# Kernel tuning notes

Hardware: AMD Instinct MI355X
Metric: run time of the kernel (lower is better)

Reference implementation:

```python
import jax, jax.numpy as jnp
import numpy as np

N = 50000   # nodes
E = 512000  # edges
D = 64      # embedding_dim
L = 4       # num_layers
ATOM_DIMS = np.array([119, 5, 12, 12, 10, 6, 6, 2, 2])  # OGB atom feature vocab sizes
BOND_DIMS = np.array([5, 6, 2])                          # OGB bond feature vocab sizes


def _ln(x, g, b, eps=1e-5):
    m = x.mean(-1, keepdims=True)
    v = x.var(-1, keepdims=True)
    return (x - m) * jax.lax.rsqrt(v + eps) * g + b


def setup_inputs() -> dict:
    key = jax.random.key(0)
    ks = jax.random.split(key, 12)
    s = 0.05
    x = jax.random.randint(ks[0], (N, 9), 0, jnp.asarray(ATOM_DIMS)[None, :])
    edge_attr = jax.random.randint(ks[1], (E, 3), 0, jnp.asarray(BOND_DIMS)[None, :])
    edge_index = jax.random.randint(ks[2], (2, E), 0, N)
    # padded embedding tables: [n_feats, max_vocab, D]
    atom_emb = jax.random.normal(ks[3], (9, 119, D), jnp.float32) * s
    bond_emb = jax.random.normal(ks[4], (3, 6, D), jnp.float32) * s
    eps = jnp.zeros((L,), jnp.float32)  # GIN eps, init 0
    W1 = jax.random.normal(ks[5], (L, D, 2 * D), jnp.float32) * s
    b1 = jnp.zeros((L, 2 * D), jnp.float32)
    W2 = jax.random.normal(ks[6], (L, 2 * D, D), jnp.float32) * s
    b2 = jnp.zeros((L, D), jnp.float32)
    ln_g = jnp.ones((L, D), jnp.float32)
    ln_b = jnp.zeros((L, D), jnp.float32)
    Wu1 = jax.random.normal(ks[7], (L, 3 * D, 3 * D), jnp.float32) * s
    bu1 = jnp.zeros((L, 3 * D), jnp.float32)
    ug = jnp.ones((L, 3 * D), jnp.float32)
    ub = jnp.zeros((L, 3 * D), jnp.float32)
    Wu2 = jax.random.normal(ks[8], (L, 3 * D, D), jnp.float32) * s
    bu2 = jnp.zeros((L, D), jnp.float32)
    return dict(x=x, edge_attr=edge_attr, edge_index=edge_index,
                atom_emb=atom_emb, bond_emb=bond_emb, eps=eps,
                W1=W1, b1=b1, W2=W2, b2=b2, ln_g=ln_g, ln_b=ln_b,
                Wu1=Wu1, bu1=bu1, ug=ug, ub=ub, Wu2=Wu2, bu2=bu2)


def reference(x, edge_attr, edge_index, atom_emb, bond_emb, eps,
              W1, b1, W2, b2, ln_g, ln_b, Wu1, bu1, ug, ub, Wu2, bu2):
    # Atom/Bond encoders: sum of per-column categorical embeddings
    node = atom_emb[jnp.arange(9)[None, :], x].sum(axis=1)       # [N, D]
    edge = bond_emb[jnp.arange(3)[None, :], edge_attr].sum(axis=1)  # [E, D]
    src, dst = edge_index[0], edge_index[1]
    for l in range(L):
        # MyGINConv (GINE): aggregate relu(x_src + e) at dst, mlp((1+eps)x + agg)
        msg = jax.nn.relu(node[src] + edge)                      # [E, D]
        agg = jax.ops.segment_sum(msg, dst, num_segments=N)      # [N, D]
        h = (1.0 + eps[l]) * node + agg
        h = jax.nn.relu(h @ W1[l] + b1[l]) @ W2[l] + b2[l]       # conv MLP
        h = _ln(h, ln_g[l], ln_b[l])                             # batch_norms[l] (LayerNorm)
        node = jax.nn.relu(h) + node                             # dropout=identity (eval) + residual
        # SparseEdgeUpdateLayer (residual=True)
        cat = jnp.concatenate([node[src], node[dst], edge], axis=-1)  # [E, 3D]
        m = _ln(cat @ Wu1[l] + bu1[l], ug[l], ub[l])
        edge = jax.nn.relu(m) @ Wu2[l] + bu2[l] + edge
    return node, edge
```

## Files before the change

### kernel.cpp

```cpp
#include <hip/hip_runtime.h>
#include <hip/hip_bf16.h>


#define GIN_N 50000
#define GIN_E 512000

typedef __attribute__((ext_vector_type(8))) short short8;
typedef __attribute__((ext_vector_type(4))) float f32x4;
typedef unsigned short u16;

__device__ __forceinline__ u16 bf16r(float x) {
    unsigned u = __builtin_bit_cast(unsigned, x);
    u += 0x7fffu + ((u >> 16) & 1u);
    return (u16)(u >> 16);
}
__device__ __forceinline__ float bf16f(u16 h) {
    unsigned u = ((unsigned)h) << 16;
    return __builtin_bit_cast(float, u);
}

__global__ __launch_bounds__(256) void zero_f32(float* __restrict__ p, int n) {
    int i = blockIdx.x * 256 + threadIdx.x;
    if (i < n) p[i] = 0.f;
}

__global__ __launch_bounds__(256) void atom_encode(const int* __restrict__ x,
        const float* __restrict__ emb, float* __restrict__ node, int N) {
    int idx = blockIdx.x * 256 + threadIdx.x;
    int n = idx >> 6, lane = idx & 63;
    if (n >= N) return;
    float s = 0.f;
#pragma unroll
    for (int f = 0; f < 9; ++f) {
        int v = x[n * 9 + f];
        s += emb[(f * 119 + v) * 64 + lane];
    }
    node[(size_t)n * 64 + lane] = s;
}

__global__ __launch_bounds__(256) void bond_encode(const int* __restrict__ ea,
        const float* __restrict__ emb, float* __restrict__ edge, int E) {
    int idx = blockIdx.x * 256 + threadIdx.x;
    int e = idx >> 6, lane = idx & 63;
    if (e >= E) return;
    float s = 0.f;
#pragma unroll
    for (int f = 0; f < 3; ++f) {
        int v = ea[e * 3 + f];
        s += emb[(f * 6 + v) * 64 + lane];
    }
    edge[(size_t)e * 64 + lane] = s;
}

__global__ __launch_bounds__(256) void msg_scatter(const int* __restrict__ src,
        const int* __restrict__ dst, const float* __restrict__ node,
        const float* __restrict__ edge, float* __restrict__ agg, int E) {
    int idx = blockIdx.x * 256 + threadIdx.x;
    int e = idx >> 6, lane = idx & 63;
    if (e >= E) return;
    int s = src[e], d = dst[e];
    float v = node[(size_t)s * 64 + lane] + edge[(size_t)e * 64 + lane];
    v = fmaxf(v, 0.f);
    unsafeAtomicAdd(&agg[(size_t)d * 64 + lane], v);
}

__global__ __launch_bounds__(256) void pack_b1(const float* __restrict__ W,
        u16* __restrict__ out, int K, int Nc, int F) {
    int tid = blockIdx.x * 256 + threadIdx.x;
    int lane = tid & 63;
    int frag = (tid >> 6) % F;
    int layer = tid / (F * 64);
    int tpr = Nc / 16;
    int ks = frag / tpr, tt = frag % tpr;
    int k0 = ks * 32 + ((lane >> 4) << 3);
    int col = tt * 16 + (lane & 15);
    const float* w = W + (size_t)layer * K * Nc;
    u16* o = out + ((size_t)layer * F + frag) * 512 + (size_t)lane * 8;
#pragma unroll
    for (int j = 0; j < 8; ++j) o[j] = bf16r(w[(size_t)(k0 + j) * Nc + col]);
}
__global__ __launch_bounds__(256) void pack_b2(const float* __restrict__ W,
        u16* __restrict__ out, int K, int Nc, int F) {
    int tid = blockIdx.x * 256 + threadIdx.x;
    int lane = tid & 63;
    int frag = (tid >> 6) % F;
    int layer = tid / (F * 64);
    int tpr = Nc / 16;
    int ks = frag / tpr, tt = frag % tpr;
    int k0 = ks * 32 + ((lane >> 4) << 3);
    int col = tt * 16 + (lane & 15);
    const float* w = W + (size_t)layer * K * Nc;
    u16* o = out + ((size_t)layer * F + frag) * 1024 + (size_t)lane * 8;
#pragma unroll
    for (int j = 0; j < 8; ++j) {
        float v = w[(size_t)(k0 + j) * Nc + col];
        u16 hi = bf16r(v);
        o[j] = hi;
        o[512 + j] = bf16r(v - bf16f(hi));
    }
}

__global__ __launch_bounds__(256, 2) void node_mlp(
        const float* __restrict__ nodeIn, float* __restrict__ nodeOut,
        float* __restrict__ agg,
        const float* __restrict__ epsArr, int l,
        const u16* __restrict__ pw1, const u16* __restrict__ pw2,
        const float* __restrict__ b1, const float* __restrict__ b2,
        const float* __restrict__ lng, const float* __restrict__ lnb, int N) {
    __shared__ u16 xH[64][72], xL[64][72];
    __shared__ u16 hH[64][136], hL[64][136];
    __shared__ float pS[4][64], pS2[4][64], lnM[64], lnR[64];
    const int t = threadIdx.x, w = t >> 6, lane = t & 63;
    const int g = lane >> 4, c0 = lane & 15;
    const float epf = 1.f + epsArr[l];

#pragma unroll
    for (int i = 0; i < 16; ++i) {
        int r = w * 16 + i;
        int n = blockIdx.x * 64 + r;
        float x = 0.f;
        if (n < N) {
            size_t o = (size_t)n * 64 + lane;
            x = epf * nodeIn[o] + agg[o];
            agg[o] = 0.f;
        }
        u16 h = bf16r(x);
        xH[r][lane] = h;
        xL[r][lane] = bf16r(x - bf16f(h));
    }
    __syncthreads();

    f32x4 a1[4][2];
#pragma unroll
    for (int sp = 0; sp < 4; ++sp)
#pragma unroll
        for (int lt = 0; lt < 2; ++lt) a1[sp][lt] = (f32x4)0.f;
#pragma unroll
    for (int ks = 0; ks < 2; ++ks) {
        short8 aH[4], aL[4];
#pragma unroll
        for (int sp = 0; sp < 4; ++sp) {
            aH[sp] = *(const short8*)&xH[sp * 16 + c0][ks * 32 + g * 8];
            aL[sp] = *(const short8*)&xL[sp * 16 + c0][ks * 32 + g * 8];
        }
#pragma unroll
        for (int lt = 0; lt < 2; ++lt) {
            const u16* p = pw1 + (size_t)(ks * 8 + w * 2 + lt) * 1024 + (size_t)lane * 8;
            short8 bH = *(const short8*)p;
            short8 bL = *(const short8*)(p + 512);
#pragma unroll
            for (int sp = 0; sp < 4; ++sp) {
                a1[sp][lt] = __builtin_amdgcn_mfma_f32_16x16x32_bf16(aH[sp], bH, a1[sp][lt], 0, 0, 0);
                a1[sp][lt] = __builtin_amdgcn_mfma_f32_16x16x32_bf16(aH[sp], bL, a1[sp][lt], 0, 0, 0);
                a1[sp][lt] = __builtin_amdgcn_mfma_f32_16x16x32_bf16(aL[sp], bH, a1[sp][lt], 0, 0, 0);
            }
        }
    }
#pragma unroll
    for (int lt = 0; lt < 2; ++lt) {
        int col = w * 32 + lt * 16 + c0;
        float bias = b1[col];
#pragma unroll
        for (int sp = 0; sp < 4; ++sp)
#pragma unroll
            for (int rg = 0; rg < 4; ++rg) {
                int r = sp * 16 + g * 4 + rg;
                float v = fmaxf(a1[sp][lt][rg] + bias, 0.f);
                u16 h = bf16r(v);
                hH[r][col] = h;
                hL[r][col] = bf16r(v - bf16f(h));
            }
    }
    __syncthreads();

    f32x4 a2[4];
#pragma unroll
    for (int sp = 0; sp < 4; ++sp) a2[sp] = (f32x4)0.f;
#pragma unroll
    for (int ks = 0; ks < 4; ++ks) {
        const u16* p = pw2 + (size_t)(ks * 4 + w) * 1024 + (size_t)lane * 8;
        short8 bH = *(const short8*)p;
        short8 bL = *(const short8*)(p + 512);
#pragma unroll
        for (int sp = 0; sp < 4; ++sp) {
            short8 aH = *(const short8*)&hH[sp * 16 + c0][ks * 32 + g * 8];
            short8 aL = *(const short8*)&hL[sp * 16 + c0][ks * 32 + g * 8];
            a2[sp] = __builtin_amdgcn_mfma_f32_16x16x32_bf16(aH, bH, a2[sp], 0, 0, 0);
            a2[sp] = __builtin_amdgcn_mfma_f32_16x16x32_bf16(aH, bL, a2[sp], 0, 0, 0);
            a2[sp] = __builtin_amdgcn_mfma_f32_16x16x32_bf16(aL, bH, a2[sp], 0, 0, 0);
        }
    }
    float bias2 = b2[w * 16 + c0];
    float s1v[4][4], s2v[4][4];
#pragma unroll
    for (int sp = 0; sp < 4; ++sp)
#pragma unroll
        for (int rg = 0; rg < 4; ++rg) {
            float v = a2[sp][rg] + bias2;
            a2[sp][rg] = v;
            s1v[sp][rg] = v;
            s2v[sp][rg] = v * v;
        }
#pragma unroll
    for (int off = 1; off < 16; off <<= 1)
#pragma unroll
        for (int sp = 0; sp < 4; ++sp)
#pragma unroll
            for (int rg = 0; rg < 4; ++rg) {
                s1v[sp][rg] += __shfl_xor(s1v[sp][rg], off);
                s2v[sp][rg] += __shfl_xor(s2v[sp][rg], off);
            }
    if (c0 == 0) {
#pragma unroll
        for (int sp = 0; sp < 4; ++sp)
#pragma unroll
            for (int rg = 0; rg < 4; ++rg) {
                int r = sp * 16 + g * 4 + rg;
                pS[w][r] = s1v[sp][rg];
                pS2[w][r] = s2v[sp][rg];
            }
    }
    __syncthreads();
    if (t < 64) {
        float a = pS[0][t] + pS[1][t] + pS[2][t] + pS[3][t];
        float b = pS2[0][t] + pS2[1][t] + pS2[2][t] + pS2[3][t];
        float mean = a * (1.f / 64.f);
        float var = b * (1.f / 64.f) - mean * mean;
        lnM[t] = mean;
        lnR[t] = rsqrtf(var + 1e-5f);
    }
    __syncthreads();

    int col = w * 16 + c0;
    float gg = lng[col], bc = lnb[col];
#pragma unroll
    for (int sp = 0; sp < 4; ++sp)
#pragma unroll
        for (int rg = 0; rg < 4; ++rg) {
            int r = sp * 16 + g * 4 + rg;
            int n = blockIdx.x * 64 + r;
            if (n < N) {
                float y = (a2[sp][rg] - lnM[r]) * lnR[r] * gg + bc;
                float xold = nodeIn[(size_t)n * 64 + col];
                nodeOut[(size_t)n * 64 + col] = fmaxf(y, 0.f) + xold;
            }
        }
}

template <bool SCATTER>
__global__ __launch_bounds__(256, 4) void edge_update_v4(
        const int* __restrict__ src, const int* __restrict__ dst,
        const float* __restrict__ node, float* __restrict__ edge,
        float* __restrict__ agg,
        const u16* __restrict__ pb1, const u16* __restrict__ pb2,
        const float* __restrict__ bu1, const float* __restrict__ ug,
        const float* __restrict__ ub, const float* __restrict__ bu2) {
    __shared__ u16 cat[64][200];
    __shared__ float pS[4][64], pS2[4][64];
    __shared__ float lnM[64], lnR[64];
    const int t = threadIdx.x, w = t >> 6, lane = t & 63;
    const int g = lane >> 4, c0 = lane & 15;
    const long eB = (long)blockIdx.x * 64;

#pragma unroll
    for (int i = 0; i < 16; ++i) {
        int r = w * 16 + i;
        long ge = eB + r;
        int s = src[ge], d = dst[ge];
        cat[r][lane]       = bf16r(node[(size_t)s * 64 + lane]);
        cat[r][64 + lane]  = bf16r(node[(size_t)d * 64 + lane]);
        cat[r][128 + lane] = bf16r(edge[(size_t)ge * 64 + lane]);
    }
    __syncthreads();

    f32x4 acc[4][3];
#pragma unroll
    for (int sp = 0; sp < 4; ++sp)
#pragma unroll
        for (int lt = 0; lt < 3; ++lt) acc[sp][lt] = (f32x4)0.f;
#pragma unroll
    for (int ks = 0; ks < 6; ++ks) {
        short8 a[4];
#pragma unroll
        for (int sp = 0; sp < 4; ++sp)
            a[sp] = *(const short8*)&cat[sp * 16 + c0][ks * 32 + g * 8];
#pragma unroll
        for (int lt = 0; lt < 3; ++lt) {
            const u16* p = pb1 + (size_t)(ks * 12 + w * 3 + lt) * 512 + (size_t)lane * 8;
            short8 b = *(const short8*)p;
#pragma unroll
            for (int sp = 0; sp < 4; ++sp)
                acc[sp][lt] = __builtin_amdgcn_mfma_f32_16x16x32_bf16(a[sp], b, acc[sp][lt], 0, 0, 0);
        }
    }

    float bs[3];
#pragma unroll
    for (int lt = 0; lt < 3; ++lt) bs[lt] = bu1[w * 48 + lt * 16 + c0];
    float s1v[4][4], s2v[4][4];
#pragma unroll
    for (int sp = 0; sp < 4; ++sp)
#pragma unroll
        for (int rg = 0; rg < 4; ++rg) { s1v[sp][rg] = 0.f; s2v[sp][rg] = 0.f; }
#pragma unroll
    for (int sp = 0; sp < 4; ++sp)
#pragma unroll
        for (int lt = 0; lt < 3; ++lt)
#pragma unroll
            for (int rg = 0; rg < 4; ++rg) {
                float v = acc[sp][lt][rg] + bs[lt];
                acc[sp][lt][rg] = v;
                s1v[sp][rg] += v;
                s2v[sp][rg] += v * v;
            }
#pragma unroll
    for (int off = 1; off < 16; off <<= 1)
#pragma unroll
        for (int sp = 0; sp < 4; ++sp)
#pragma unroll
            for (int rg = 0; rg < 4; ++rg) {
                s1v[sp][rg] += __shfl_xor(s1v[sp][rg], off);
                s2v[sp][rg] += __shfl_xor(s2v[sp][rg], off);
            }
    if (c0 == 0) {
#pragma unroll
        for (int sp = 0; sp < 4; ++sp)
#pragma unroll
            for (int rg = 0; rg < 4; ++rg) {
                int r = sp * 16 + g * 4 + rg;
                pS[w][r] = s1v[sp][rg];
                pS2[w][r] = s2v[sp][rg];
            }
    }
    __syncthreads();
    if (t < 64) {
        float a = pS[0][t] + pS[1][t] + pS[2][t] + pS[3][t];
        float b = pS2[0][t] + pS2[1][t] + pS2[2][t] + pS2[3][t];
        float mean = a * (1.f / 192.f);
        float var = b * (1.f / 192.f) - mean * mean;
        lnM[t] = mean;
        lnR[t] = rsqrtf(var + 1e-5f);
    }
    __syncthreads();

#pragma unroll
    for (int lt = 0; lt < 3; ++lt) {
        int col = w * 48 + lt * 16 + c0;
        float gg = ug[col], bb = ub[col];
#pragma unroll
        for (int sp = 0; sp < 4; ++sp)
#pragma unroll
            for (int rg = 0; rg < 4; ++rg) {
                int r = sp * 16 + g * 4 + rg;
                float v = (acc[sp][lt][rg] - lnM[r]) * lnR[r] * gg + bb;
                cat[r][col] = bf16r(fmaxf(v, 0.f));
            }
    }
    __syncthreads();

    f32x4 a2[4];
#pragma unroll
    for (int sp = 0; sp < 4; ++sp) a2[sp] = (f32x4)0.f;
#pragma unroll
    for (int ks = 0; ks < 6; ++ks) {
        const u16* p = pb2 + (size_t)(ks * 4 + w) * 512 + (size_t)lane * 8;
        short8 b = *(const short8*)p;
#pragma unroll
        for (int sp = 0; sp < 4; ++sp) {
            short8 a = *(const short8*)&cat[sp * 16 + c0][ks * 32 + g * 8];
            a2[sp] = __builtin_amdgcn_mfma_f32_16x16x32_bf16(a, b, a2[sp], 0, 0, 0);
        }
    }
    const int col = w * 16 + c0;
    float bb2 = bu2[col];
#pragma unroll
    for (int sp = 0; sp < 4; ++sp)
#pragma unroll
        for (int rg = 0; rg < 4; ++rg) {
            int r = sp * 16 + g * 4 + rg;
            long ge = eB + r;
            size_t off = (size_t)ge * 64 + col;
            float eNew = a2[sp][rg] + bb2 + edge[off];
            edge[off] = eNew;
            if (SCATTER) {
                int s = src[ge];
                float ns = node[(size_t)s * 64 + col];
                float msg = fmaxf(ns + eNew, 0.f);
                int dd = dst[ge];
                unsafeAtomicAdd(&agg[(size_t)dd * 64 + col], msg);
            }
        }
}

extern "C" void kernel_launch(void* const* d_in, const int* in_sizes, int n_in,
                              void* d_out, int out_size, void* d_ws, size_t ws_size,
                              hipStream_t stream) {
    const int*   x         = (const int*)d_in[0];
    const int*   edge_attr = (const int*)d_in[1];
    const int*   edge_index= (const int*)d_in[2];
    const float* atom_emb  = (const float*)d_in[3];
    const float* bond_emb  = (const float*)d_in[4];
    const float* eps       = (const float*)d_in[5];
    const float* W1        = (const float*)d_in[6];
    const float* b1        = (const float*)d_in[7];
    const float* W2        = (const float*)d_in[8];
    const float* b2        = (const float*)d_in[9];
    const float* ln_g      = (const float*)d_in[10];
    const float* ln_b      = (const float*)d_in[11];
    const float* Wu1       = (const float*)d_in[12];
    const float* bu1       = (const float*)d_in[13];
    const float* ug        = (const float*)d_in[14];
    const float* ub        = (const float*)d_in[15];
    const float* Wu2       = (const float*)d_in[16];
    const float* bu2       = (const float*)d_in[17];

    const int N = GIN_N, E = GIN_E;
    const int* src = edge_index;
    const int* dst = edge_index + E;

    float* node = (float*)d_out;
    float* edge = (float*)d_out + (size_t)N * 64;

    char* ws = (char*)d_ws;
    float* nodeAlt = (float*)ws;  ws += (size_t)N * 64 * 4;
    float* agg     = (float*)ws;  ws += (size_t)N * 64 * 4;
    u16* pb1       = (u16*)ws;    ws += (size_t)4 * 72 * 512 * 2;
    u16* pb2       = (u16*)ws;    ws += (size_t)4 * 24 * 512 * 2;
    u16* pw1       = (u16*)ws;    ws += (size_t)4 * 16 * 1024 * 2;
    u16* pw2       = (u16*)ws;    ws += (size_t)4 * 16 * 1024 * 2;

    pack_b1<<<(4 * 72 * 64) / 256, 256, 0, stream>>>(Wu1, pb1, 192, 192, 72);
    pack_b1<<<(4 * 24 * 64) / 256, 256, 0, stream>>>(Wu2, pb2, 192, 64, 24);
    pack_b2<<<(4 * 16 * 64) / 256, 256, 0, stream>>>(W1, pw1, 64, 128, 16);
    pack_b2<<<(4 * 16 * 64) / 256, 256, 0, stream>>>(W2, pw2, 128, 64, 16);

    atom_encode<<<(N * 64 + 255) / 256, 256, 0, stream>>>(x, atom_emb, node, N);
    bond_encode<<<(E * 64) / 256, 256, 0, stream>>>(edge_attr, bond_emb, edge, E);

    zero_f32<<<(N * 64) / 256, 256, 0, stream>>>(agg, N * 64);
    msg_scatter<<<(E * 64) / 256, 256, 0, stream>>>(src, dst, node, edge, agg, E);

    const int nodeBlocks = (N + 63) / 64;
    for (int l = 0; l < 4; ++l) {
        const float* nIn  = (l & 1) ? nodeAlt : node;
        float*       nOut = (l & 1) ? node    : nodeAlt;
        node_mlp<<<nodeBlocks, 256, 0, stream>>>(nIn, nOut, agg, eps, l,
            pw1 + (size_t)l * 16 * 1024, pw2 + (size_t)l * 16 * 1024,
            b1 + (size_t)l * 128, b2 + (size_t)l * 64,
            ln_g + (size_t)l * 64, ln_b + (size_t)l * 64, N);
        if (l < 3)
            edge_update_v4<true><<<E / 64, 256, 0, stream>>>(src, dst, nOut, edge, agg,
                pb1 + (size_t)l * 72 * 512, pb2 + (size_t)l * 24 * 512,
                bu1 + (size_t)l * 192,
                ug + (size_t)l * 192, ub + (size_t)l * 192,
                bu2 + (size_t)l * 64);
        else
            edge_update_v4<false><<<E / 64, 256, 0, stream>>>(src, dst, nOut, edge, agg,
                pb1 + (size_t)l * 72 * 512, pb2 + (size_t)l * 24 * 512,
                bu1 + (size_t)l * 192,
                ug + (size_t)l * 192, ub + (size_t)l * 192,
                bu2 + (size_t)l * 64);
    }
}
```

Baseline: 989.2 us.

## Restructure edge update to per-wave 16-edge tiles with bf16 node copy

Each wave now owns 16 edges and computes all 192 columns of the first GEMM itself. A-fragments are loaded straight from global memory into registers, and LayerNorm statistics come from lane shuffles. This removes the shared-memory staging of the concatenated inputs and all block-wide __syncthreads. The node MLP additionally writes a bf16 copy of node features so the edge gathers read half the bytes. The bond encoder is also fused with the initial message scatter, saving one pass over the edge tensor. The trade-off is that each wave re-reads the whole Wu1 fragment set, and more accumulator registers are live per wave, which may lower occupancy.

After: 1.043 ms. 5.4% more time.

```diff
diff --git a/kernel.cpp b/kernel.cpp
--- a/kernel.cpp
+++ b/kernel.cpp
@@ -17,6 +17,14 @@
 __device__ __forceinline__ float bf16f(u16 h) {
     unsigned u = ((unsigned)h) << 16;
     return __builtin_bit_cast(float, u);
+}
+__device__ __forceinline__ short8 cvt8(float4 u, float4 v) {
+    short8 r;
+    r[0] = (short)bf16r(u.x); r[1] = (short)bf16r(u.y);
+    r[2] = (short)bf16r(u.z); r[3] = (short)bf16r(u.w);
+    r[4] = (short)bf16r(v.x); r[5] = (short)bf16r(v.y);
+    r[6] = (short)bf16r(v.z); r[7] = (short)bf16r(v.w);
+    return r;
 }
 
 __global__ __launch_bounds__(256) void zero_f32(float* __restrict__ p, int n) {
@@ -38,8 +46,11 @@
     node[(size_t)n * 64 + lane] = s;
 }
 
-__global__ __launch_bounds__(256) void bond_encode(const int* __restrict__ ea,
-        const float* __restrict__ emb, float* __restrict__ edge, int E) {
+__global__ __launch_bounds__(256) void bond_encode_scatter(
+        const int* __restrict__ ea, const float* __restrict__ emb,
+        float* __restrict__ edge, const int* __restrict__ src,
+        const int* __restrict__ dst, const float* __restrict__ node,
+        float* __restrict__ agg, int E) {
     int idx = blockIdx.x * 256 + threadIdx.x;
     int e = idx >> 6, lane = idx & 63;
     if (e >= E) return;
@@ -50,18 +61,9 @@
         s += emb[(f * 6 + v) * 64 + lane];
     }
     edge[(size_t)e * 64 + lane] = s;
-}
-
-__global__ __launch_bounds__(256) void msg_scatter(const int* __restrict__ src,
-        const int* __restrict__ dst, const float* __restrict__ node,
-        const float* __restrict__ edge, float* __restrict__ agg, int E) {
-    int idx = blockIdx.x * 256 + threadIdx.x;
-    int e = idx >> 6, lane = idx & 63;
-    if (e >= E) return;
-    int s = src[e], d = dst[e];
-    float v = node[(size_t)s * 64 + lane] + edge[(size_t)e * 64 + lane];
-    v = fmaxf(v, 0.f);
-    unsafeAtomicAdd(&agg[(size_t)d * 64 + lane], v);
+    int si = src[e], di = dst[e];
+    float msg = fmaxf(node[(size_t)si * 64 + lane] + s, 0.f);
+    unsafeAtomicAdd(&agg[(size_t)di * 64 + lane], msg);
 }
 
 __global__ __launch_bounds__(256) void pack_b1(const float* __restrict__ W,
@@ -102,7 +104,7 @@
 
 __global__ __launch_bounds__(256, 2) void node_mlp(
         const float* __restrict__ nodeIn, float* __restrict__ nodeOut,
-        float* __restrict__ agg,
+        u16* __restrict__ nodeB, float* __restrict__ agg,
         const float* __restrict__ epsArr, int l,
         const u16* __restrict__ pw1, const u16* __restrict__ pw2,
         const float* __restrict__ b1, const float* __restrict__ b2,
@@ -242,154 +244,129 @@
             if (n < N) {
                 float y = (a2[sp][rg] - lnM[r]) * lnR[r] * gg + bc;
                 float xold = nodeIn[(size_t)n * 64 + col];
-                nodeOut[(size_t)n * 64 + col] = fmaxf(y, 0.f) + xold;
+                float out = fmaxf(y, 0.f) + xold;
+                nodeOut[(size_t)n * 64 + col] = out;
+                nodeB[(size_t)n * 64 + col] = bf16r(out);
             }
         }
 }
 
 template <bool SCATTER>
-__global__ __launch_bounds__(256, 4) void edge_update_v4(
+__global__ __launch_bounds__(256, 4) void edge_update_v5(
         const int* __restrict__ src, const int* __restrict__ dst,
-        const float* __restrict__ node, float* __restrict__ edge,
-        float* __restrict__ agg,
+        const float* __restrict__ node, const u16* __restrict__ nodeB,
+        float* __restrict__ edge, float* __restrict__ agg,
         const u16* __restrict__ pb1, const u16* __restrict__ pb2,
         const float* __restrict__ bu1, const float* __restrict__ ug,
         const float* __restrict__ ub, const float* __restrict__ bu2) {
-    __shared__ u16 cat[64][200];
-    __shared__ float pS[4][64], pS2[4][64];
-    __shared__ float lnM[64], lnR[64];
+    __shared__ u16 mld[4][16][200];
     const int t = threadIdx.x, w = t >> 6, lane = t & 63;
     const int g = lane >> 4, c0 = lane & 15;
-    const long eB = (long)blockIdx.x * 64;
-
-#pragma unroll
-    for (int i = 0; i < 16; ++i) {
-        int r = w * 16 + i;
-        long ge = eB + r;
-        int s = src[ge], d = dst[ge];
-        cat[r][lane]       = bf16r(node[(size_t)s * 64 + lane]);
-        cat[r][64 + lane]  = bf16r(node[(size_t)d * 64 + lane]);
-        cat[r][128 + lane] = bf16r(edge[(size_t)ge * 64 + lane]);
-    }
-    __syncthreads();
-
-    f32x4 acc[4][3];
-#pragma unroll
-    for (int sp = 0; sp < 4; ++sp)
-#pragma unroll
-        for (int lt = 0; lt < 3; ++lt) acc[sp][lt] = (f32x4)0.f;
+    const int eB16 = (blockIdx.x * 4 + w) * 16;
+
+    const int eRow = eB16 + c0;
+    const int sI = src[eRow], dI = dst[eRow];
+    const u16* nsrow = nodeB + (size_t)sI * 64;
+    const u16* ndrow = nodeB + (size_t)dI * 64;
+    const float* erow = edge + (size_t)eRow * 64;
+    short8 a[6];
+    a[0] = *(const short8*)(nsrow + g * 8);
+    a[1] = *(const short8*)(nsrow + 32 + g * 8);
+    a[2] = *(const short8*)(ndrow + g * 8);
+    a[3] = *(const short8*)(ndrow + 32 + g * 8);
+    {
+        float4 e0 = *(const float4*)(erow + g * 8);
+        float4 e1 = *(const float4*)(erow + g * 8 + 4);
+        float4 e2 = *(const float4*)(erow + 32 + g * 8);
+        float4 e3 = *(const float4*)(erow + 32 + g * 8 + 4);
+        a[4] = cvt8(e0, e1);
+        a[5] = cvt8(e2, e3);
+    }
+
+    f32x4 acc1[12];
+#pragma unroll
+    for (int lt = 0; lt < 12; ++lt) acc1[lt] = (f32x4)0.f;
+#pragma unroll
+    for (int lt = 0; lt < 12; ++lt) {
+#pragma unroll
+        for (int ks = 0; ks < 6; ++ks) {
+            const u16* p = pb1 + (size_t)(ks * 12 + lt) * 512 + (size_t)lane * 8;
+            short8 b = *(const short8*)p;
+            acc1[lt] = __builtin_amdgcn_mfma_f32_16x16x32_bf16(a[ks], b, acc1[lt], 0, 0, 0);
+        }
+    }
+
+    float s1[4] = {0.f, 0.f, 0.f, 0.f}, s2[4] = {0.f, 0.f, 0.f, 0.f};
+#pragma unroll
+    for (int lt = 0; lt < 12; ++lt) {
+        float bias = bu1[lt * 16 + c0];
+#pragma unroll
+        for (int rg = 0; rg < 4; ++rg) {
+            float v = acc1[lt][rg] + bias;
+            acc1[lt][rg] = v;
+            s1[rg] += v;
+            s2[rg] += v * v;
+        }
+    }
+#pragma unroll
+    for (int off = 1; off < 16; off <<= 1)
+#pragma unroll
+        for (int rg = 0; rg < 4; ++rg) {
+            s1[rg] += __shfl_xor(s1[rg], off);
+            s2[rg] += __shfl_xor(s2[rg], off);
+        }
+    float mean[4], rs[4];
+#pragma unroll
+    for (int rg = 0; rg < 4; ++rg) {
+        mean[rg] = s1[rg] * (1.f / 192.f);
+        float var = s2[rg] * (1.f / 192.f) - mean[rg] * mean[rg];
+        rs[rg] = rsqrtf(var + 1e-5f);
+    }
+
+#pragma unroll
+    for (int lt = 0; lt < 12; ++lt) {
+        int col = lt * 16 + c0;
+        float gg = ug[col], bb = ub[col];
+#pragma unroll
+        for (int rg = 0; rg < 4; ++rg) {
+            float v = (acc1[lt][rg] - mean[rg]) * rs[rg] * gg + bb;
+            mld[w][g * 4 + rg][col] = bf16r(fmaxf(v, 0.f));
+        }
+    }
+    asm volatile("s_waitcnt lgkmcnt(0)" ::: "memory");
+    __builtin_amdgcn_sched_barrier(0);
+
+    f32x4 acc2[4];
+#pragma unroll
+    for (int lt = 0; lt < 4; ++lt) acc2[lt] = (f32x4)0.f;
 #pragma unroll
     for (int ks = 0; ks < 6; ++ks) {
-        short8 a[4];
-#pragma unroll
-        for (int sp = 0; sp < 4; ++sp)
-            a[sp] = *(const short8*)&cat[sp * 16 + c0][ks * 32 + g * 8];
-#pragma unroll
-        for (int lt = 0; lt < 3; ++lt) {
-            const u16* p = pb1 + (size_t)(ks * 12 + w * 3 + lt) * 512 + (size_t)lane * 8;
+        short8 av = *(const short8*)&mld[w][c0][ks * 32 + g * 8];
+#pragma unroll
+        for (int lt = 0; lt < 4; ++lt) {
+            const u16* p = pb2 + (size_t)(ks * 4 + lt) * 512 + (size_t)lane * 8;
             short8 b = *(const short8*)p;
-#pragma unroll
-            for (int sp = 0; sp < 4; ++sp)
-                acc[sp][lt] = __builtin_amdgcn_mfma_f32_16x16x32_bf16(a[sp], b, acc[sp][lt], 0, 0, 0);
-        }
-    }
-
-    float bs[3];
-#pragma unroll
-    for (int lt = 0; lt < 3; ++lt) bs[lt] = bu1[w * 48 + lt * 16 + c0];
-    float s1v[4][4], s2v[4][4];
-#pragma unroll
-    for (int sp = 0; sp < 4; ++sp)
-#pragma unroll
-        for (int rg = 0; rg < 4; ++rg) { s1v[sp][rg] = 0.f; s2v[sp][rg] = 0.f; }
-#pragma unroll
-    for (int sp = 0; sp < 4; ++sp)
-#pragma unroll
-        for (int lt = 0; lt < 3; ++lt)
-#pragma unroll
-            for (int rg = 0; rg < 4; ++rg) {
-                float v = acc[sp][lt][rg] + bs[lt];
-                acc[sp][lt][rg] = v;
-                s1v[sp][rg] += v;
-                s2v[sp][rg] += v * v;
-            }
-#pragma unroll
-    for (int off = 1; off < 16; off <<= 1)
-#pragma unroll
-        for (int sp = 0; sp < 4; ++sp)
-#pragma unroll
-            for (int rg = 0; rg < 4; ++rg) {
-                s1v[sp][rg] += __shfl_xor(s1v[sp][rg], off);
-                s2v[sp][rg] += __shfl_xor(s2v[sp][rg], off);
-            }
-    if (c0 == 0) {
-#pragma unroll
-        for (int sp = 0; sp < 4; ++sp)
-#pragma unroll
-            for (int rg = 0; rg < 4; ++rg) {
-                int r = sp * 16 + g * 4 + rg;
-                pS[w][r] = s1v[sp][rg];
-                pS2[w][r] = s2v[sp][rg];
-            }
-    }
-    __syncthreads();
-    if (t < 64) {
-        float a = pS[0][t] + pS[1][t] + pS[2][t] + pS[3][t];
-        float b = pS2[0][t] + pS2[1][t] + pS2[2][t] + pS2[3][t];
-        float mean = a * (1.f / 192.f);
-        float var = b * (1.f / 192.f) - mean * mean;
-        lnM[t] = mean;
-        lnR[t] = rsqrtf(var + 1e-5f);
-    }
-    __syncthreads();
-
-#pragma unroll
-    for (int lt = 0; lt < 3; ++lt) {
-        int col = w * 48 + lt * 16 + c0;
-        float gg = ug[col], bb = ub[col];
-#pragma unroll
-        for (int sp = 0; sp < 4; ++sp)
-#pragma unroll
-            for (int rg = 0; rg < 4; ++rg) {
-                int r = sp * 16 + g * 4 + rg;
-                float v = (acc[sp][lt][rg] - lnM[r]) * lnR[r] * gg + bb;
-                cat[r][col] = bf16r(fmaxf(v, 0.f));
-            }
-    }
-    __syncthreads();
-
-    f32x4 a2[4];
-#pragma unroll
-    for (int sp = 0; sp < 4; ++sp) a2[sp] = (f32x4)0.f;
-#pragma unroll
-    for (int ks = 0; ks < 6; ++ks) {
-        const u16* p = pb2 + (size_t)(ks * 4 + w) * 512 + (size_t)lane * 8;
-        short8 b = *(const short8*)p;
-#pragma unroll
-        for (int sp = 0; sp < 4; ++sp) {
-            short8 a = *(const short8*)&cat[sp * 16 + c0][ks * 32 + g * 8];
-            a2[sp] = __builtin_amdgcn_mfma_f32_16x16x32_bf16(a, b, a2[sp], 0, 0, 0);
-        }
-    }
-    const int col = w * 16 + c0;
-    float bb2 = bu2[col];
-#pragma unroll
-    for (int sp = 0; sp < 4; ++sp)
-#pragma unroll
-        for (int rg = 0; rg < 4; ++rg) {
-            int r = sp * 16 + g * 4 + rg;
-            long ge = eB + r;
-            size_t off = (size_t)ge * 64 + col;
-            float eNew = a2[sp][rg] + bb2 + edge[off];
+            acc2[lt] = __builtin_amdgcn_mfma_f32_16x16x32_bf16(av, b, acc2[lt], 0, 0, 0);
+        }
+    }
+
+#pragma unroll
+    for (int rg = 0; rg < 4; ++rg) {
+        int e = eB16 + g * 4 + rg;
+        int sI2 = 0, dI2 = 0;
+        if (SCATTER) { sI2 = src[e]; dI2 = dst[e]; }
+#pragma unroll
+        for (int lt = 0; lt < 4; ++lt) {
+            int col = lt * 16 + c0;
+            size_t off = (size_t)e * 64 + col;
+            float eNew = acc2[lt][rg] + bu2[col] + edge[off];
             edge[off] = eNew;
             if (SCATTER) {
-                int s = src[ge];
-                float ns = node[(size_t)s * 64 + col];
-                float msg = fmaxf(ns + eNew, 0.f);
-                int dd = dst[ge];
-                unsafeAtomicAdd(&agg[(size_t)dd * 64 + col], msg);
-            }
-        }
+                float msg = fmaxf(node[(size_t)sI2 * 64 + col] + eNew, 0.f);
+                unsafeAtomicAdd(&agg[(size_t)dI2 * 64 + col], msg);
+            }
+        }
+    }
 }
 
 extern "C" void kernel_launch(void* const* d_in, const int* in_sizes, int n_in,
@@ -424,6 +401,7 @@
     char* ws = (char*)d_ws;
     float* nodeAlt = (float*)ws;  ws += (size_t)N * 64 * 4;
     float* agg     = (float*)ws;  ws += (size_t)N * 64 * 4;
+    u16*   nodeB   = (u16*)ws;    ws += (size_t)N * 64 * 2;
     u16* pb1       = (u16*)ws;    ws += (size_t)4 * 72 * 512 * 2;
     u16* pb2       = (u16*)ws;    ws += (size_t)4 * 24 * 512 * 2;
     u16* pw1       = (u16*)ws;    ws += (size_t)4 * 16 * 1024 * 2;
@@ -435,27 +413,28 @@
     pack_b2<<<(4 * 16 * 64) / 256, 256, 0, stream>>>(W2, pw2, 128, 64, 16);
 
     atom_encode<<<(N * 64 + 255) / 256, 256, 0, stream>>>(x, atom_emb, node, N);
-    bond_encode<<<(E * 64) / 256, 256, 0, stream>>>(edge_attr, bond_emb, edge, E);
-
     zero_f32<<<(N * 64) / 256, 256, 0, stream>>>(agg, N * 64);
-    msg_scatter<<<(E * 64) / 256, 256, 0, stream>>>(src, dst, node, edge, agg, E);
+    bond_encode_scatter<<<(E * 64) / 256, 256, 0, stream>>>(edge_attr, bond_emb,
+        edge, src, dst, node, agg, E);
 
     const int nodeBlocks = (N + 63) / 64;
     for (int l = 0; l < 4; ++l) {
         const float* nIn  = (l & 1) ? nodeAlt : node;
         float*       nOut = (l & 1) ? node    : nodeAlt;
-        node_mlp<<<nodeBlocks, 256, 0, stream>>>(nIn, nOut, agg, eps, l,
+        node_mlp<<<nodeBlocks, 256, 0, stream>>>(nIn, nOut, nodeB, agg, eps, l,
             pw1 + (size_t)l * 16 * 1024, pw2 + (size_t)l * 16 * 1024,
             b1 + (size_t)l * 128, b2 + (size_t)l * 64,
             ln_g + (size_t)l * 64, ln_b + (size_t)l * 64, N);
         if (l < 3)
-            edge_update_v4<true><<<E / 64, 256, 0, stream>>>(src, dst, nOut, edge, agg,
+            edge_update_v5<true><<<E / 64, 256, 0, stream>>>(src, dst, nOut, nodeB,
+                edge, agg,
                 pb1 + (size_t)l * 72 * 512, pb2 + (size_t)l * 24 * 512,
                 bu1 + (size_t)l * 192,
                 ug + (size_t)l * 192, ub + (size_t)l * 192,
                 bu2 + (size_t)l * 64);
         else
-            edge_update_v4<false><<<E / 64, 256, 0, stream>>>(src, dst, nOut, edge, agg,
+            edge_update_v5<false><<<E / 64, 256, 0, stream>>>(src, dst, nOut, nodeB,
+                edge, agg,
                 pb1 + (size_t)l * 72 * 512, pb2 + (size_t)l * 24 * 512,
                 bu1 + (size_t)l * 192,
                 ug + (size_t)l * 192, ub + (size_t)l * 192,
```

## Store edge and node state in bf16 and fuse bond encode with first scatter

Applied to the files above, without the earlier changes.

Keeps the running edge embedding in a bf16 workspace buffer and writes the fp32 edge output only in the last layer. Node_mlp also writes a bf16 copy of the node state so the edge kernel gathers 2-byte rows instead of converting fp32. Bond encoding is fused with the first message scatter, and the node ping-pong buffer is replaced by in-place updates. This roughly halves gather and edge read/write traffic. The cost is that the residual edge path now accumulates in bf16 across layers, which loses precision relative to the fp32 reference.

New measurement: 912.7 us. 1.08x faster.

```diff
diff --git a/kernel.cpp b/kernel.cpp
--- a/kernel.cpp
+++ b/kernel.cpp
@@ -38,8 +38,11 @@
     node[(size_t)n * 64 + lane] = s;
 }
 
-__global__ __launch_bounds__(256) void bond_encode(const int* __restrict__ ea,
-        const float* __restrict__ emb, float* __restrict__ edge, int E) {
+__global__ __launch_bounds__(256) void bond_encode_scatter(
+        const int* __restrict__ ea, const float* __restrict__ emb,
+        u16* __restrict__ edgeB, const int* __restrict__ src,
+        const int* __restrict__ dst, const float* __restrict__ node,
+        float* __restrict__ agg, int E) {
     int idx = blockIdx.x * 256 + threadIdx.x;
     int e = idx >> 6, lane = idx & 63;
     if (e >= E) return;
@@ -49,19 +52,10 @@
         int v = ea[e * 3 + f];
         s += emb[(f * 6 + v) * 64 + lane];
     }
-    edge[(size_t)e * 64 + lane] = s;
-}
-
-__global__ __launch_bounds__(256) void msg_scatter(const int* __restrict__ src,
-        const int* __restrict__ dst, const float* __restrict__ node,
-        const float* __restrict__ edge, float* __restrict__ agg, int E) {
-    int idx = blockIdx.x * 256 + threadIdx.x;
-    int e = idx >> 6, lane = idx & 63;
-    if (e >= E) return;
-    int s = src[e], d = dst[e];
-    float v = node[(size_t)s * 64 + lane] + edge[(size_t)e * 64 + lane];
-    v = fmaxf(v, 0.f);
-    unsafeAtomicAdd(&agg[(size_t)d * 64 + lane], v);
+    edgeB[(size_t)e * 64 + lane] = bf16r(s);
+    int si = src[e], di = dst[e];
+    float msg = fmaxf(node[(size_t)si * 64 + lane] + s, 0.f);
+    unsafeAtomicAdd(&agg[(size_t)di * 64 + lane], msg);
 }
 
 __global__ __launch_bounds__(256) void pack_b1(const float* __restrict__ W,
@@ -101,7 +95,7 @@
 }
 
 __global__ __launch_bounds__(256, 2) void node_mlp(
-        const float* __restrict__ nodeIn, float* __restrict__ nodeOut,
+        float* __restrict__ node, u16* __restrict__ nodeB,
         float* __restrict__ agg,
         const float* __restrict__ epsArr, int l,
         const u16* __restrict__ pw1, const u16* __restrict__ pw2,
@@ -121,7 +115,7 @@
         float x = 0.f;
         if (n < N) {
             size_t o = (size_t)n * 64 + lane;
-            x = epf * nodeIn[o] + agg[o];
+            x = epf * node[o] + agg[o];
             agg[o] = 0.f;
         }
         u16 h = bf16r(x);
@@ -240,22 +234,26 @@
             int r = sp * 16 + g * 4 + rg;
             int n = blockIdx.x * 64 + r;
             if (n < N) {
+                size_t o = (size_t)n * 64 + col;
                 float y = (a2[sp][rg] - lnM[r]) * lnR[r] * gg + bc;
-                float xold = nodeIn[(size_t)n * 64 + col];
-                nodeOut[(size_t)n * 64 + col] = fmaxf(y, 0.f) + xold;
+                float out = fmaxf(y, 0.f) + node[o];
+                node[o] = out;
+                nodeB[o] = bf16r(out);
             }
         }
 }
 
 template <bool SCATTER>
-__global__ __launch_bounds__(256, 4) void edge_update_v4(
+__global__ __launch_bounds__(256, 4) void edge_update_v6(
         const int* __restrict__ src, const int* __restrict__ dst,
-        const float* __restrict__ node, float* __restrict__ edge,
+        const float* __restrict__ node, const u16* __restrict__ nodeB,
+        u16* __restrict__ edgeB, float* __restrict__ edgeF,
         float* __restrict__ agg,
         const u16* __restrict__ pb1, const u16* __restrict__ pb2,
         const float* __restrict__ bu1, const float* __restrict__ ug,
         const float* __restrict__ ub, const float* __restrict__ bu2) {
-    __shared__ u16 cat[64][200];
+    __shared__ u16 cat[64][202];
+    __shared__ u16 eold[64][66];
     __shared__ float pS[4][64], pS2[4][64];
     __shared__ float lnM[64], lnR[64];
     const int t = threadIdx.x, w = t >> 6, lane = t & 63;
@@ -267,9 +265,11 @@
         int r = w * 16 + i;
         long ge = eB + r;
         int s = src[ge], d = dst[ge];
-        cat[r][lane]       = bf16r(node[(size_t)s * 64 + lane]);
-        cat[r][64 + lane]  = bf16r(node[(size_t)d * 64 + lane]);
-        cat[r][128 + lane] = bf16r(edge[(size_t)ge * 64 + lane]);
+        cat[r][lane]       = nodeB[(size_t)s * 64 + lane];
+        cat[r][64 + lane]  = nodeB[(size_t)d * 64 + lane];
+        u16 ev = edgeB[(size_t)ge * 64 + lane];
+        cat[r][128 + lane] = ev;
+        eold[r][lane] = ev;
     }
     __syncthreads();
 
@@ -371,23 +371,23 @@
             a2[sp] = __builtin_amdgcn_mfma_f32_16x16x32_bf16(a, b, a2[sp], 0, 0, 0);
         }
     }
+
     const int col = w * 16 + c0;
-    float bb2 = bu2[col];
+    const float bb2 = bu2[col];
 #pragma unroll
     for (int sp = 0; sp < 4; ++sp)
 #pragma unroll
         for (int rg = 0; rg < 4; ++rg) {
             int r = sp * 16 + g * 4 + rg;
             long ge = eB + r;
-            size_t off = (size_t)ge * 64 + col;
-            float eNew = a2[sp][rg] + bb2 + edge[off];
-            edge[off] = eNew;
+            float eNew = a2[sp][rg] + bb2 + bf16f(eold[r][col]);
             if (SCATTER) {
-                int s = src[ge];
-                float ns = node[(size_t)s * 64 + col];
-                float msg = fmaxf(ns + eNew, 0.f);
-                int dd = dst[ge];
-                unsafeAtomicAdd(&agg[(size_t)dd * 64 + col], msg);
+                edgeB[(size_t)ge * 64 + col] = bf16r(eNew);
+                int s2 = src[ge], d2 = dst[ge];
+                float msg = fmaxf(node[(size_t)s2 * 64 + col] + eNew, 0.f);
+                unsafeAtomicAdd(&agg[(size_t)d2 * 64 + col], msg);
+            } else {
+                edgeF[(size_t)ge * 64 + col] = eNew;
             }
         }
 }
@@ -418,16 +418,17 @@
     const int* src = edge_index;
     const int* dst = edge_index + E;
 
-    float* node = (float*)d_out;
-    float* edge = (float*)d_out + (size_t)N * 64;
+    float* node  = (float*)d_out;
+    float* edgeF = (float*)d_out + (size_t)N * 64;
 
     char* ws = (char*)d_ws;
-    float* nodeAlt = (float*)ws;  ws += (size_t)N * 64 * 4;
-    float* agg     = (float*)ws;  ws += (size_t)N * 64 * 4;
-    u16* pb1       = (u16*)ws;    ws += (size_t)4 * 72 * 512 * 2;
-    u16* pb2       = (u16*)ws;    ws += (size_t)4 * 24 * 512 * 2;
-    u16* pw1       = (u16*)ws;    ws += (size_t)4 * 16 * 1024 * 2;
-    u16* pw2       = (u16*)ws;    ws += (size_t)4 * 16 * 1024 * 2;
+    float* agg   = (float*)ws;  ws += (size_t)N * 64 * 4;
+    u16*   nodeB = (u16*)ws;    ws += (size_t)N * 64 * 2;
+    u16*   edgeB = (u16*)ws;    ws += (size_t)E * 64 * 2;
+    u16* pb1     = (u16*)ws;    ws += (size_t)4 * 72 * 512 * 2;
+    u16* pb2     = (u16*)ws;    ws += (size_t)4 * 24 * 512 * 2;
+    u16* pw1     = (u16*)ws;    ws += (size_t)4 * 16 * 1024 * 2;
+    u16* pw2     = (u16*)ws;    ws += (size_t)4 * 16 * 1024 * 2;
 
     pack_b1<<<(4 * 72 * 64) / 256, 256, 0, stream>>>(Wu1, pb1, 192, 192, 72);
     pack_b1<<<(4 * 24 * 64) / 256, 256, 0, stream>>>(Wu2, pb2, 192, 64, 24);
@@ -435,27 +436,26 @@
     pack_b2<<<(4 * 16 * 64) / 256, 256, 0, stream>>>(W2, pw2, 128, 64, 16);
 
     atom_encode<<<(N * 64 + 255) / 256, 256, 0, stream>>>(x, atom_emb, node, N);
-    bond_encode<<<(E * 64) / 256, 256, 0, stream>>>(edge_attr, bond_emb, edge, E);
-
     zero_f32<<<(N * 64) / 256, 256, 0, stream>>>(agg, N * 64);
-    msg_scatter<<<(E * 64) / 256, 256, 0, stream>>>(src, dst, node, edge, agg, E);
+    bond_encode_scatter<<<(E * 64) / 256, 256, 0, stream>>>(edge_attr, bond_emb,
+        edgeB, src, dst, node, agg, E);
 
     const int nodeBlocks = (N + 63) / 64;
     for (int l = 0; l < 4; ++l) {
-        const float* nIn  = (l & 1) ? nodeAlt : node;
-        float*       nOut = (l & 1) ? node    : nodeAlt;
-        node_mlp<<<nodeBlocks, 256, 0, stream>>>(nIn, nOut, agg, eps, l,
+        node_mlp<<<nodeBlocks, 256, 0, stream>>>(node, nodeB, agg, eps, l,
             pw1 + (size_t)l * 16 * 1024, pw2 + (size_t)l * 16 * 1024,
             b1 + (size_t)l * 128, b2 + (size_t)l * 64,
             ln_g + (size_t)l * 64, ln_b + (size_t)l * 64, N);
         if (l < 3)
-            edge_update_v4<true><<<E / 64, 256, 0, stream>>>(src, dst, nOut, edge, agg,
+            edge_update_v6<true><<<E / 64, 256, 0, stream>>>(src, dst, node, nodeB,
+                edgeB, edgeF, agg,
                 pb1 + (size_t)l * 72 * 512, pb2 + (size_t)l * 24 * 512,
                 bu1 + (size_t)l * 192,
                 ug + (size_t)l * 192, ub + (size_t)l * 192,
                 bu2 + (size_t)l * 64);
         else
-            edge_update_v4<false><<<E / 64, 256, 0, stream>>>(src, dst, nOut, edge, agg,
+            edge_update_v6<false><<<E / 64, 256, 0, stream>>>(src, dst, node, nodeB,
+                edgeB, edgeF, agg,
                 pb1 + (size_t)l * 72 * 512, pb2 + (size_t)l * 24 * 512,
                 bu1 + (size_t)l * 192,
                 ug + (size_t)l * 192, ub + (size_t)l * 192,
```
